# Performance work log

Hardware: AMD Instinct MI355X
Metric: run time of the kernel (lower is better)

## Reference

```python
import jax, jax.numpy as jnp
import numpy as np

T = 36
N_POLES = 40
LAM = 0.1
MAX_ITER = 100
TOL = 1e-4
B, P = 2, 4096


def build_dictionary(Drr, Dtheta):
    # rows i = 0..T-1; columns: [rr^i cos(i th), (-rr)^i cos(i th), rr^i sin(i th), (-rr)^i sin(i th)]
    i = jnp.arange(T, dtype=Drr.dtype)[:, None]              # [T,1]
    pr = jnp.power(Drr[None, :], i)                          # rr^i   [T,N]
    sign = jnp.power(jnp.asarray(-1.0, Drr.dtype), i)        # (-1)^i [T,1]
    c = jnp.cos(i * Dtheta[None, :])
    s = jnp.sin(i * Dtheta[None, :])
    dic = jnp.concatenate([pr * c, sign * pr * c, pr * s, sign * pr * s], axis=1)  # [T,4N]
    G = jnp.linalg.norm(dic, axis=0)                         # column norms
    G = jnp.where(G == 0, jnp.sqrt(jnp.asarray(float(T), dic.dtype)), G)
    return dic / G


def soft_shrink(v, lambd):
    return jnp.sign(v) * jnp.maximum(jnp.abs(v) - lambd, 0.0)


def fista(D, Y, lam, max_iter=MAX_ITER):
    DtD = D.T @ D                                            # [4N,4N]
    L = jnp.linalg.norm(DtD)                                 # torch.norm(DtD, 2) = Frobenius norm
    linv = 1.0 / L
    DtY = jnp.einsum('tk,btp->bkp', D, Y) * linv             # [B,4N,P]
    K = DtD.shape[0]
    A = jnp.eye(K, dtype=D.dtype) - DtD * linv               # [4N,4N]
    lambd = lam * linv
    Bb, _, Pp = DtY.shape

    # FISTA momentum coefficients are data independent -> precompute
    ts = np.ones(max_iter + 1)
    for k in range(max_iter):
        ts[k + 1] = (1 + np.sqrt(1 + 4 * ts[k] ** 2)) / 2.0
    tts = jnp.asarray((ts[:-1] - 1) / ts[1:], dtype=D.dtype)  # [max_iter]

    x0 = jnp.zeros((Bb, K, Pp), dtype=D.dtype)

    def step(carry, inputs):
        x_old, y_old, done = carry
        tt, k = inputs
        x_new = soft_shrink(jnp.einsum('kj,bjp->bkp', A, y_old) + DtY, lambd)
        y_new = x_new * (1 + tt) - x_old * tt
        # torch divides by x_old.shape[1]: P on the first check (x_old is the 2-D zeros init), 4N after
        denom = jnp.where(k == 0, float(Pp), float(K)).astype(x_new.dtype)
        conv = jnp.linalg.norm(x_old - x_new) / denom < TOL
        x_out = jnp.where(done, x_old, x_new)
        y_out = jnp.where(done, y_old, y_new)
        return (x_out, y_out, jnp.logical_or(done, conv)), None

    (x_fin, _, _), _ = jax.lax.scan(step, (x0, x0, jnp.array(False)),
                                    (tts, jnp.arange(max_iter)))
    return x_fin


def setup_inputs() -> dict:
    key = jax.random.key(0)
    k1, k2, k3 = jax.random.split(key, 3)
    Drr = jax.random.uniform(k1, (N_POLES,), dtype=jnp.float32)
    Dtheta = jax.random.uniform(k2, (N_POLES,), dtype=jnp.float32)
    x = jax.random.normal(k3, (B, T, P), dtype=jnp.float32)
    return {"Drr": Drr, "Dtheta": Dtheta, "x": x}


def reference(Drr, Dtheta, x):
    dic = build_dictionary(Drr, Dtheta)   # [T, 4N]
    sparsecode = fista(dic, x, LAM)       # [B, 4N, P]
    return sparsecode
```

## Files before the change

kernel.cpp:

```cpp
#include <hip/hip_runtime.h>
#include <hip/hip_fp16.h>

#define TT 36
#define KK 160
#define NPOLE 40
#define PP 4096
#define MAXIT 100
#define COLS 16
#define NG 2
#define NWC 4
#define NTHR 512
#define YS 168
#define GRID 256

#define WS_TTS   2
#define WS_ROWN  160
#define WS_D     512
#define WS_A     6400

typedef float    floatx4 __attribute__((ext_vector_type(4)));
typedef _Float16 halfx8  __attribute__((ext_vector_type(8)));

__global__ __launch_bounds__(256)
void setup_kernel(const float* __restrict__ Drr, const float* __restrict__ Dth,
                  float* __restrict__ ws) {
  __shared__ float Dl[TT * KK];
  __shared__ float red[256];
  const int a = blockIdx.x, tid = threadIdx.x;

  if (tid < KK) {
    int gg = tid / NPOLE, n = tid % NPOLE;
    float rr = Drr[n], th = Dth[n];
    float srr = (gg & 1) ? -rr : rr;
    float sth, cth; __sincosf(th, &sth, &cth);
    float c = 1.f, s = 0.f, pr = 1.f, ss = 0.f;
    for (int t = 0; t < TT; t++) {
      float val = pr * ((gg < 2) ? c : s);
      Dl[t * KK + tid] = val;
      ss = fmaf(val, val, ss);
      float cn = c * cth - s * sth;
      float sn = s * cth + c * sth;
      c = cn; s = sn; pr *= srr;
    }
    float gn = sqrtf(ss);
    gn = (gn == 0.f) ? sqrtf((float)TT) : gn;
    float inv = 1.f / gn;
    for (int t = 0; t < TT; t++) Dl[t * KK + tid] *= inv;
  }
  if (a == 0 && tid == 0) {
    double ts = 1.0;
    for (int k = 0; k < MAXIT; k++) {
      double tn = (1.0 + sqrt(1.0 + 4.0 * ts * ts)) * 0.5;
      ws[WS_TTS + k] = (float)((ts - 1.0) / tn);
      ts = tn;
    }
  }
  __syncthreads();

  if (a == 0)
    for (int idx = tid; idx < TT * KK; idx += 256) ws[WS_D + idx] = Dl[idx];

  float ss2 = 0.f;
  if (tid < KK) {
    float s2 = 0.f;
    for (int t = 0; t < TT; t++) s2 = fmaf(Dl[t * KK + a], Dl[t * KK + tid], s2);
    ws[WS_A + a * KK + tid] = s2;
    ss2 = s2 * s2;
  }
  red[tid] = ss2;
  __syncthreads();
  for (int off = 128; off > 0; off >>= 1) {
    if (tid < off) red[tid] += red[tid + off];
    __syncthreads();
  }
  if (tid == 0) ws[WS_ROWN + a] = red[0];
}

__global__ __launch_bounds__(NTHR, 2)
void fista_kernel(const float* __restrict__ x, float* __restrict__ out,
                  const float* __restrict__ ws) {
  __shared__ __align__(16) short ys[NG][2][COLS * YS];
  __shared__ float ttsl[MAXIT];
  __shared__ unsigned cnt[NG];

  const int tid  = threadIdx.x;
  const int w    = tid >> 6;
  const int lane = tid & 63;
  const int quad = lane >> 4;
  const int l16  = lane & 15;
  const int g    = w >> 2;
  const int v    = w & 3;
  const int bid  = blockIdx.x;
  const int bb   = (bid * 32) / PP;
  const int p0   = (bid * 32) % PP + 16 * g;

  float frob = 0.f;
  {
    const float* rn = &ws[WS_ROWN];
#pragma unroll
    for (int i = 0; i < KK; i += 4) {
      float4 r4 = *(const float4*)&rn[i];
      frob += ((r4.x + r4.y) + r4.z) + r4.w;
    }
  }
  const float linv  = 1.0f / sqrtf(frob);
  const float lambd = 0.1f * linv;
  const float adiag = 1.0f - linv;
  const float ahf   = (float)(_Float16)adiag;
  const float ddiag = adiag - ahf;

  int base, nrs;
  if (g == 0) { base = (v < 2) ? 48 * v : 32 * v + 32; nrs = (v < 2) ? 3 : 2; }
  else        { base = (v < 2) ? 32 * v : 48 * v - 32; nrs = (v < 2) ? 2 : 3; }

  for (int i = tid; i < MAXIT; i += NTHR) ttsl[i] = ws[WS_TTS + i];

  const float* DtDw = &ws[WS_A];
  halfx8 ah[3][5];
#pragma unroll
  for (int rs = 0; rs < 3; rs++) {
    if (rs < nrs) {
      const int myrow = base + 16 * rs + l16;
      const float* rowp = &DtDw[myrow * KK];
#pragma unroll
      for (int kc = 0; kc < 5; kc++) {
        float4 d0 = *(const float4*)&rowp[32 * kc + 8 * quad];
        float4 d1 = *(const float4*)&rowp[32 * kc + 8 * quad + 4];
        float vals[8] = {d0.x, d0.y, d0.z, d0.w, d1.x, d1.y, d1.z, d1.w};
        union { halfx8 v8; _Float16 h8[8]; } fr;
#pragma unroll
        for (int e = 0; e < 8; e++) {
          int kpos = 32 * kc + 8 * quad + e;
          float aval = (kpos == myrow) ? adiag : (-vals[e] * linv);
          fr.h8[e] = (_Float16)aval;
        }
        ah[rs][kc] = fr.v8;
      }
    }
  }

  const float* Dg = &ws[WS_D];
  float dty[3][4] = {{0.f,0.f,0.f,0.f},{0.f,0.f,0.f,0.f},{0.f,0.f,0.f,0.f}};
  {
    const float* xcol = &x[(size_t)bb * TT * PP + p0 + l16];
    for (int t = 0; t < TT; t++) {
      float xv = xcol[(size_t)t * PP];
#pragma unroll
      for (int rs = 0; rs < 3; rs++) {
        if (rs < nrs) {
          float4 d = *(const float4*)&Dg[t * KK + base + 16 * rs + 4 * quad];
          dty[rs][0] = fmaf(d.x, xv, dty[rs][0]);
          dty[rs][1] = fmaf(d.y, xv, dty[rs][1]);
          dty[rs][2] = fmaf(d.z, xv, dty[rs][2]);
          dty[rs][3] = fmaf(d.w, xv, dty[rs][3]);
        }
      }
    }
#pragma unroll
    for (int rs = 0; rs < 3; rs++)
#pragma unroll
      for (int r = 0; r < 4; r++) dty[rs][r] *= linv;
  }

  {
    int* z = (int*)&ys[0][0][0];
    for (int i = tid; i < NG * 2 * COLS * YS / 2; i += NTHR) z[i] = 0;
    if (tid < NG) cnt[tid] = 0;
  }
  float xo[3][4] = {{0.f,0.f,0.f,0.f},{0.f,0.f,0.f,0.f},{0.f,0.f,0.f,0.f}};
  float yl[3][4] = {{0.f,0.f,0.f,0.f},{0.f,0.f,0.f,0.f},{0.f,0.f,0.f,0.f}};
  float yv[3][4] = {{0.f,0.f,0.f,0.f},{0.f,0.f,0.f,0.f},{0.f,0.f,0.f,0.f}};
  __syncthreads();

  if (g == 1) __builtin_amdgcn_s_sleep(10);
  __builtin_amdgcn_s_setprio(1);

#define RD_MFMA(KC) { \
    halfx8 bh = *(const halfx8*)&yb[cb + 32 * (KC)]; \
    _Pragma("unroll") \
    for (int rs = 0; rs < 3; rs++) \
      if (rs < nrs) \
        accM[rs] = __builtin_amdgcn_mfma_f32_16x16x32_f16(ah[rs][KC], bh, accM[rs], 0, 0, 0); \
  }

#define ITER_BODY(SK, K1, K2, K3, K4) { \
    RD_MFMA(SK) \
    if (it > 0) { \
      const unsigned tgt = (unsigned)(NWC * it); \
      __builtin_amdgcn_s_setprio(0); \
      while (__atomic_load_n(&cnt[g], __ATOMIC_ACQUIRE) < tgt) \
        __builtin_amdgcn_s_sleep(1); \
      __builtin_amdgcn_s_setprio(1); \
    } \
    RD_MFMA(K1) RD_MFMA(K2) RD_MFMA(K3) RD_MFMA(K4) \
  }

  for (int it = 0; it < MAXIT; it++) {
    const short* yb = &ys[g][it & 1][0];
    const int cb = l16 * YS + 8 * quad;
    floatx4 accM[3] = {{dty[0][0], dty[0][1], dty[0][2], dty[0][3]},
                       {dty[1][0], dty[1][1], dty[1][2], dty[1][3]},
                       {dty[2][0], dty[2][1], dty[2][2], dty[2][3]}};

    if (g == 0) {
      if      (v == 0) ITER_BODY(0, 1, 2, 3, 4)
      else if (v == 1) ITER_BODY(2, 0, 1, 3, 4)
      else if (v == 2) ITER_BODY(3, 0, 1, 2, 4)
      else             ITER_BODY(4, 0, 1, 2, 3)
    } else {
      if      (v == 0) ITER_BODY(0, 1, 2, 3, 4)
      else if (v == 1) ITER_BODY(1, 0, 2, 3, 4)
      else if (v == 2) ITER_BODY(2, 0, 1, 3, 4)
      else             ITER_BODY(4, 0, 1, 2, 3)
    }

    const float tt = ttsl[it];
    short* yw = &ys[g][(it & 1) ^ 1][0];
#pragma unroll
    for (int rs = 0; rs < 3; rs++) {
      if (rs < nrs) {
        float yn[4];
#pragma unroll
        for (int r = 0; r < 4; r++) {
          float vv = fmaf(ddiag, yv[rs][r], fmaf(ahf, yl[rs][r], accM[rs][r]));
          float cl = __builtin_amdgcn_fmed3f(vv, -lambd, lambd);
          float xv = vv - cl;
          yn[r] = fmaf(tt, xv - xo[rs][r], xv);
          xo[rs][r] = xv;
        }
        _Float16 h0 = (_Float16)yn[0], h1 = (_Float16)yn[1];
        _Float16 h2 = (_Float16)yn[2], h3 = (_Float16)yn[3];
        yl[rs][0] = yn[0] - (float)h0;  yv[rs][0] = yn[0];
        yl[rs][1] = yn[1] - (float)h1;  yv[rs][1] = yn[1];
        yl[rs][2] = yn[2] - (float)h2;  yv[rs][2] = yn[2];
        yl[rs][3] = yn[3] - (float)h3;  yv[rs][3] = yn[3];
        unsigned u01 = (unsigned)__builtin_bit_cast(unsigned short, h0) |
                       ((unsigned)__builtin_bit_cast(unsigned short, h1) << 16);
        unsigned u23 = (unsigned)__builtin_bit_cast(unsigned short, h2) |
                       ((unsigned)__builtin_bit_cast(unsigned short, h3) << 16);
        const int ko = l16 * YS + base + 16 * rs + 4 * quad;
        *(uint2*)&yw[ko] = make_uint2(u01, u23);
      }
    }

    if (lane == 0) __atomic_fetch_add(&cnt[g], 1u, __ATOMIC_RELEASE);
  }

#pragma unroll
  for (int rs = 0; rs < 3; rs++) {
    if (rs < nrs) {
#pragma unroll
      for (int r = 0; r < 4; r++)
        out[((size_t)bb * KK + base + 16 * rs + 4 * quad + r) * PP + p0 + l16] = xo[rs][r];
    }
  }
}

extern "C" void kernel_launch(void* const* d_in, const int* in_sizes, int n_in,
                              void* d_out, int out_size, void* d_ws, size_t ws_size,
                              hipStream_t stream) {
  const float* Drr = (const float*)d_in[0];
  const float* Dth = (const float*)d_in[1];
  const float* x   = (const float*)d_in[2];
  float* out = (float*)d_out;
  float* ws  = (float*)d_ws;
  (void)in_sizes; (void)n_in; (void)out_size; (void)ws_size;

  setup_kernel<<<160, 256, 0, stream>>>(Drr, Dth, ws);
  fista_kernel<<<GRID, NTHR, 0, stream>>>(x, out, ws);
}
```

Measured before the change: 171.7 us.

## Fuse dictionary and Gram setup into FISTA kernel with MFMA Gram computation

Removes the separate setup kernel and its global workspace round-trip. Each block now builds the dictionary in shared memory and computes D^T D with split hi/lo fp16 MFMAs. It derives the Frobenius norm from that product, and the momentum coefficients are passed as a host-computed kernel argument. The iteration is reformulated to keep raw DtD (zero diagonal) in fp16, apply the diagonal term in fp32, and drop the fp16 residual (yl) correction of y. Every block repeats the setup work, the much larger shared-memory footprint may cut blocks per CU, and accuracy may shift.

```diff
diff --git a/kernel.cpp b/kernel.cpp
--- a/kernel.cpp
+++ b/kernel.cpp
@@ -1,5 +1,6 @@
 #include <hip/hip_runtime.h>
 #include <hip/hip_fp16.h>
+#include <cmath>
 
 #define TT 36
 #define KK 160
@@ -12,76 +13,44 @@
 #define NTHR 512
 #define YS 168
 #define GRID 256
-
-#define WS_TTS   2
-#define WS_ROWN  160
-#define WS_D     512
-#define WS_A     6400
+#define TW 64
+#define AW 168
+
+#define OFF_TH 23040
+#define OFF_TL 43520
+#define OFF_A  64000
+#define SM_SZ  117760
 
 typedef float    floatx4 __attribute__((ext_vector_type(4)));
 typedef _Float16 halfx8  __attribute__((ext_vector_type(8)));
 
-__global__ __launch_bounds__(256)
-void setup_kernel(const float* __restrict__ Drr, const float* __restrict__ Dth,
-                  float* __restrict__ ws) {
-  __shared__ float Dl[TT * KK];
-  __shared__ float red[256];
-  const int a = blockIdx.x, tid = threadIdx.x;
-
-  if (tid < KK) {
-    int gg = tid / NPOLE, n = tid % NPOLE;
-    float rr = Drr[n], th = Dth[n];
-    float srr = (gg & 1) ? -rr : rr;
-    float sth, cth; __sincosf(th, &sth, &cth);
-    float c = 1.f, s = 0.f, pr = 1.f, ss = 0.f;
-    for (int t = 0; t < TT; t++) {
-      float val = pr * ((gg < 2) ? c : s);
-      Dl[t * KK + tid] = val;
-      ss = fmaf(val, val, ss);
-      float cn = c * cth - s * sth;
-      float sn = s * cth + c * sth;
-      c = cn; s = sn; pr *= srr;
-    }
-    float gn = sqrtf(ss);
-    gn = (gn == 0.f) ? sqrtf((float)TT) : gn;
-    float inv = 1.f / gn;
-    for (int t = 0; t < TT; t++) Dl[t * KK + tid] *= inv;
-  }
-  if (a == 0 && tid == 0) {
-    double ts = 1.0;
-    for (int k = 0; k < MAXIT; k++) {
-      double tn = (1.0 + sqrt(1.0 + 4.0 * ts * ts)) * 0.5;
-      ws[WS_TTS + k] = (float)((ts - 1.0) / tn);
-      ts = tn;
-    }
-  }
-  __syncthreads();
-
-  if (a == 0)
-    for (int idx = tid; idx < TT * KK; idx += 256) ws[WS_D + idx] = Dl[idx];
-
-  float ss2 = 0.f;
-  if (tid < KK) {
-    float s2 = 0.f;
-    for (int t = 0; t < TT; t++) s2 = fmaf(Dl[t * KK + a], Dl[t * KK + tid], s2);
-    ws[WS_A + a * KK + tid] = s2;
-    ss2 = s2 * s2;
-  }
-  red[tid] = ss2;
-  __syncthreads();
-  for (int off = 128; off > 0; off >>= 1) {
-    if (tid < off) red[tid] += red[tid + off];
-    __syncthreads();
-  }
-  if (tid == 0) ws[WS_ROWN + a] = red[0];
+struct TtsArg { float v[MAXIT]; };
+
+static TtsArg host_tts() {
+  TtsArg a;
+  double ts = 1.0;
+  for (int k = 0; k < MAXIT; k++) {
+    double tn = (1.0 + sqrt(1.0 + 4.0 * ts * ts)) * 0.5;
+    a.v[k] = (float)((ts - 1.0) / tn);
+    ts = tn;
+  }
+  return a;
 }
 
 __global__ __launch_bounds__(NTHR, 2)
-void fista_kernel(const float* __restrict__ x, float* __restrict__ out,
-                  const float* __restrict__ ws) {
-  __shared__ __align__(16) short ys[NG][2][COLS * YS];
+void fista_kernel(const float* __restrict__ Drr, const float* __restrict__ Dth,
+                  const float* __restrict__ x, float* __restrict__ out,
+                  TtsArg targ) {
+  __shared__ __align__(16) char smem[SM_SZ];
   __shared__ float ttsl[MAXIT];
+  __shared__ float red[8];
   __shared__ unsigned cnt[NG];
+
+  float*    rawD = (float*)smem;
+  _Float16* Th   = (_Float16*)(smem + OFF_TH);
+  _Float16* Tl   = (_Float16*)(smem + OFF_TL);
+  _Float16* Ah   = (_Float16*)(smem + OFF_A);
+  short*    ysb  = (short*)smem;
 
   const int tid  = threadIdx.x;
   const int w    = tid >> 6;
@@ -94,52 +63,43 @@
   const int bb   = (bid * 32) / PP;
   const int p0   = (bid * 32) % PP + 16 * g;
 
-  float frob = 0.f;
-  {
-    const float* rn = &ws[WS_ROWN];
-#pragma unroll
-    for (int i = 0; i < KK; i += 4) {
-      float4 r4 = *(const float4*)&rn[i];
-      frob += ((r4.x + r4.y) + r4.z) + r4.w;
-    }
-  }
-  const float linv  = 1.0f / sqrtf(frob);
-  const float lambd = 0.1f * linv;
-  const float adiag = 1.0f - linv;
-  const float ahf   = (float)(_Float16)adiag;
-  const float ddiag = adiag - ahf;
-
   int base, nrs;
   if (g == 0) { base = (v < 2) ? 48 * v : 32 * v + 32; nrs = (v < 2) ? 3 : 2; }
   else        { base = (v < 2) ? 32 * v : 48 * v - 32; nrs = (v < 2) ? 2 : 3; }
 
-  for (int i = tid; i < MAXIT; i += NTHR) ttsl[i] = ws[WS_TTS + i];
-
-  const float* DtDw = &ws[WS_A];
-  halfx8 ah[3][5];
-#pragma unroll
-  for (int rs = 0; rs < 3; rs++) {
-    if (rs < nrs) {
-      const int myrow = base + 16 * rs + l16;
-      const float* rowp = &DtDw[myrow * KK];
-#pragma unroll
-      for (int kc = 0; kc < 5; kc++) {
-        float4 d0 = *(const float4*)&rowp[32 * kc + 8 * quad];
-        float4 d1 = *(const float4*)&rowp[32 * kc + 8 * quad + 4];
-        float vals[8] = {d0.x, d0.y, d0.z, d0.w, d1.x, d1.y, d1.z, d1.w};
-        union { halfx8 v8; _Float16 h8[8]; } fr;
-#pragma unroll
-        for (int e = 0; e < 8; e++) {
-          int kpos = 32 * kc + 8 * quad + e;
-          float aval = (kpos == myrow) ? adiag : (-vals[e] * linv);
-          fr.h8[e] = (_Float16)aval;
-        }
-        ah[rs][kc] = fr.v8;
-      }
-    }
-  }
-
-  const float* Dg = &ws[WS_D];
+  for (int i = tid; i < MAXIT; i += NTHR) ttsl[i] = targ.v[i];
+
+  if (tid < KK) {
+    int gg = tid / NPOLE, n = tid % NPOLE;
+    float rr = Drr[n], th = Dth[n];
+    float srr = (gg & 1) ? -rr : rr;
+    float sth, cth; __sincosf(th, &sth, &cth);
+    float c = 1.f, s = 0.f, pr = 1.f, ss = 0.f;
+    for (int t = 0; t < TT; t++) {
+      float val = pr * ((gg < 2) ? c : s);
+      rawD[t * KK + tid] = val;
+      ss = fmaf(val, val, ss);
+      float cn = c * cth - s * sth;
+      float sn = s * cth + c * sth;
+      c = cn; s = sn; pr *= srr;
+    }
+    float gn = sqrtf(ss);
+    gn = (gn == 0.f) ? sqrtf((float)TT) : gn;
+    float inv = 1.f / gn;
+    for (int t = 0; t < TT; t++) {
+      float d = rawD[t * KK + tid] * inv;
+      rawD[t * KK + tid] = d;
+      _Float16 h = (_Float16)d;
+      Th[tid * TW + t] = h;
+      Tl[tid * TW + t] = (_Float16)(d - (float)h);
+    }
+    for (int t = TT; t < TW; t++) {
+      Th[tid * TW + t] = (_Float16)0.f;
+      Tl[tid * TW + t] = (_Float16)0.f;
+    }
+  }
+  __syncthreads();
+
   float dty[3][4] = {{0.f,0.f,0.f,0.f},{0.f,0.f,0.f,0.f},{0.f,0.f,0.f,0.f}};
   {
     const float* xcol = &x[(size_t)bb * TT * PP + p0 + l16];
@@ -148,7 +108,7 @@
 #pragma unroll
       for (int rs = 0; rs < 3; rs++) {
         if (rs < nrs) {
-          float4 d = *(const float4*)&Dg[t * KK + base + 16 * rs + 4 * quad];
+          float4 d = *(const float4*)&rawD[t * KK + base + 16 * rs + 4 * quad];
           dty[rs][0] = fmaf(d.x, xv, dty[rs][0]);
           dty[rs][1] = fmaf(d.y, xv, dty[rs][1]);
           dty[rs][2] = fmaf(d.z, xv, dty[rs][2]);
@@ -159,16 +119,60 @@
 #pragma unroll
     for (int rs = 0; rs < 3; rs++)
 #pragma unroll
-      for (int r = 0; r < 4; r++) dty[rs][r] *= linv;
+      for (int r = 0; r < 4; r++) dty[rs][r] = -dty[rs][r];
+  }
+
+  float fpart = 0.f;
+  for (int tix = w; tix < 100; tix += 8) {
+    int i = tix / 10, j = tix % 10;
+    floatx4 acc = {0.f, 0.f, 0.f, 0.f};
+#pragma unroll
+    for (int ks = 0; ks < 2; ks++) {
+      halfx8 Ah8 = *(const halfx8*)&Th[(16 * i + l16) * TW + 32 * ks + 8 * quad];
+      halfx8 Al8 = *(const halfx8*)&Tl[(16 * i + l16) * TW + 32 * ks + 8 * quad];
+      halfx8 Bh8 = *(const halfx8*)&Th[(16 * j + l16) * TW + 32 * ks + 8 * quad];
+      halfx8 Bl8 = *(const halfx8*)&Tl[(16 * j + l16) * TW + 32 * ks + 8 * quad];
+      acc = __builtin_amdgcn_mfma_f32_16x16x32_f16(Ah8, Bh8, acc, 0, 0, 0);
+      acc = __builtin_amdgcn_mfma_f32_16x16x32_f16(Ah8, Bl8, acc, 0, 0, 0);
+      acc = __builtin_amdgcn_mfma_f32_16x16x32_f16(Al8, Bh8, acc, 0, 0, 0);
+    }
+#pragma unroll
+    for (int r = 0; r < 4; r++) {
+      float cv = acc[r];
+      fpart += cv * cv;
+      int grow = 16 * i + 4 * quad + r, gcol = 16 * j + l16;
+      Ah[grow * AW + gcol] = (_Float16)((grow == gcol) ? 0.f : cv);
+    }
+  }
+#pragma unroll
+  for (int off = 32; off > 0; off >>= 1) fpart += __shfl_xor(fpart, off);
+  if (lane == 0) red[w] = fpart;
+  __syncthreads();
+
+  const float frob = ((((((red[0] + red[1]) + red[2]) + red[3]) + red[4])
+                       + red[5]) + red[6]) + red[7];
+  const float linv  = 1.0f / sqrtf(frob);
+  const float nlinv = -linv;
+  const float lambd = 0.1f * linv;
+  const float adiag = 1.0f - linv;
+
+  halfx8 ah[3][5];
+#pragma unroll
+  for (int rs = 0; rs < 3; rs++) {
+    if (rs < nrs) {
+      const int myrow = base + 16 * rs + l16;
+#pragma unroll
+      for (int kc = 0; kc < 5; kc++)
+        ah[rs][kc] = *(const halfx8*)&Ah[myrow * AW + 32 * kc + 8 * quad];
+    }
   }
 
   {
-    int* z = (int*)&ys[0][0][0];
+    int* z = (int*)ysb;
     for (int i = tid; i < NG * 2 * COLS * YS / 2; i += NTHR) z[i] = 0;
     if (tid < NG) cnt[tid] = 0;
   }
   float xo[3][4] = {{0.f,0.f,0.f,0.f},{0.f,0.f,0.f,0.f},{0.f,0.f,0.f,0.f}};
-  float yl[3][4] = {{0.f,0.f,0.f,0.f},{0.f,0.f,0.f,0.f},{0.f,0.f,0.f,0.f}};
   float yv[3][4] = {{0.f,0.f,0.f,0.f},{0.f,0.f,0.f,0.f},{0.f,0.f,0.f,0.f}};
   __syncthreads();
 
@@ -196,7 +200,7 @@
   }
 
   for (int it = 0; it < MAXIT; it++) {
-    const short* yb = &ys[g][it & 1][0];
+    const short* yb = ysb + (2 * g + (it & 1)) * (COLS * YS);
     const int cb = l16 * YS + 8 * quad;
     floatx4 accM[3] = {{dty[0][0], dty[0][1], dty[0][2], dty[0][3]},
                        {dty[1][0], dty[1][1], dty[1][2], dty[1][3]},
@@ -215,25 +219,22 @@
     }
 
     const float tt = ttsl[it];
-    short* yw = &ys[g][(it & 1) ^ 1][0];
+    short* yw = ysb + (2 * g + ((it & 1) ^ 1)) * (COLS * YS);
 #pragma unroll
     for (int rs = 0; rs < 3; rs++) {
       if (rs < nrs) {
         float yn[4];
 #pragma unroll
         for (int r = 0; r < 4; r++) {
-          float vv = fmaf(ddiag, yv[rs][r], fmaf(ahf, yl[rs][r], accM[rs][r]));
+          float vv = fmaf(nlinv, accM[rs][r], adiag * yv[rs][r]);
           float cl = __builtin_amdgcn_fmed3f(vv, -lambd, lambd);
           float xv = vv - cl;
           yn[r] = fmaf(tt, xv - xo[rs][r], xv);
           xo[rs][r] = xv;
+          yv[rs][r] = yn[r];
         }
         _Float16 h0 = (_Float16)yn[0], h1 = (_Float16)yn[1];
         _Float16 h2 = (_Float16)yn[2], h3 = (_Float16)yn[3];
-        yl[rs][0] = yn[0] - (float)h0;  yv[rs][0] = yn[0];
-        yl[rs][1] = yn[1] - (float)h1;  yv[rs][1] = yn[1];
-        yl[rs][2] = yn[2] - (float)h2;  yv[rs][2] = yn[2];
-        yl[rs][3] = yn[3] - (float)h3;  yv[rs][3] = yn[3];
         unsigned u01 = (unsigned)__builtin_bit_cast(unsigned short, h0) |
                        ((unsigned)__builtin_bit_cast(unsigned short, h1) << 16);
         unsigned u23 = (unsigned)__builtin_bit_cast(unsigned short, h2) |
@@ -263,9 +264,7 @@
   const float* Dth = (const float*)d_in[1];
   const float* x   = (const float*)d_in[2];
   float* out = (float*)d_out;
-  float* ws  = (float*)d_ws;
-  (void)in_sizes; (void)n_in; (void)out_size; (void)ws_size;
-
-  setup_kernel<<<160, 256, 0, stream>>>(Drr, Dth, ws);
-  fista_kernel<<<GRID, NTHR, 0, stream>>>(x, out, ws);
+  (void)d_ws; (void)ws_size; (void)in_sizes; (void)n_in; (void)out_size;
+
+  fista_kernel<<<GRID, NTHR, 0, stream>>>(Drr, Dth, x, out, host_tts());
 }
```

Measured after the change: 181.4 us. 5.7% more time.

## Precompute fp16 off-diagonal DtD, fold scaling into epilogue, pass tts as kernel arg

Applied to the files above, without the earlier changes.

Setup now stores DtD directly as fp16 with a zeroed diagonal, so the fista kernel loads A fragments without per-thread conversion. The iteration is rewritten as v = adiag*y - linv*(DtD_off*y - DtY): the diagonal is applied exactly in fp32 from the held y values, which replaces the hi/lo split compensation and drops the yl registers and several FMAs per element. The momentum coefficients are computed on the host and passed by value as a kernel argument, and buffers move from the workspace to __device__ globals. The fp16 rounding now applies to unscaled DtD entries, which changes the numerics, and the work removed from the hot loop is small.

```diff
diff --git a/kernel.cpp b/kernel.cpp
--- a/kernel.cpp
+++ b/kernel.cpp
@@ -1,5 +1,6 @@
 #include <hip/hip_runtime.h>
 #include <hip/hip_fp16.h>
+#include <cmath>
 
 #define TT 36
 #define KK 160
@@ -13,17 +14,28 @@
 #define YS 168
 #define GRID 256
 
-#define WS_TTS   2
-#define WS_ROWN  160
-#define WS_D     512
-#define WS_A     6400
-
 typedef float    floatx4 __attribute__((ext_vector_type(4)));
 typedef _Float16 halfx8  __attribute__((ext_vector_type(8)));
 
+__device__ __align__(16) float    g_D[TT * KK];
+__device__ __align__(16) float    g_rown[KK];
+__device__ __align__(16) _Float16 g_A[KK * KK];
+
+struct TtsArg { float v[MAXIT]; };
+
+static TtsArg host_tts() {
+  TtsArg a;
+  double ts = 1.0;
+  for (int k = 0; k < MAXIT; k++) {
+    double tn = (1.0 + sqrt(1.0 + 4.0 * ts * ts)) * 0.5;
+    a.v[k] = (float)((ts - 1.0) / tn);
+    ts = tn;
+  }
+  return a;
+}
+
 __global__ __launch_bounds__(256)
-void setup_kernel(const float* __restrict__ Drr, const float* __restrict__ Dth,
-                  float* __restrict__ ws) {
+void setup_kernel(const float* __restrict__ Drr, const float* __restrict__ Dth) {
   __shared__ float Dl[TT * KK];
   __shared__ float red[256];
   const int a = blockIdx.x, tid = threadIdx.x;
@@ -47,24 +59,16 @@
     float inv = 1.f / gn;
     for (int t = 0; t < TT; t++) Dl[t * KK + tid] *= inv;
   }
-  if (a == 0 && tid == 0) {
-    double ts = 1.0;
-    for (int k = 0; k < MAXIT; k++) {
-      double tn = (1.0 + sqrt(1.0 + 4.0 * ts * ts)) * 0.5;
-      ws[WS_TTS + k] = (float)((ts - 1.0) / tn);
-      ts = tn;
-    }
-  }
   __syncthreads();
 
   if (a == 0)
-    for (int idx = tid; idx < TT * KK; idx += 256) ws[WS_D + idx] = Dl[idx];
+    for (int idx = tid; idx < TT * KK; idx += 256) g_D[idx] = Dl[idx];
 
   float ss2 = 0.f;
   if (tid < KK) {
     float s2 = 0.f;
     for (int t = 0; t < TT; t++) s2 = fmaf(Dl[t * KK + a], Dl[t * KK + tid], s2);
-    ws[WS_A + a * KK + tid] = s2;
+    g_A[a * KK + tid] = (_Float16)((tid == a) ? 0.f : s2);
     ss2 = s2 * s2;
   }
   red[tid] = ss2;
@@ -73,12 +77,12 @@
     if (tid < off) red[tid] += red[tid + off];
     __syncthreads();
   }
-  if (tid == 0) ws[WS_ROWN + a] = red[0];
+  if (tid == 0) g_rown[a] = red[0];
 }
 
 __global__ __launch_bounds__(NTHR, 2)
 void fista_kernel(const float* __restrict__ x, float* __restrict__ out,
-                  const float* __restrict__ ws) {
+                  TtsArg targ) {
   __shared__ __align__(16) short ys[NG][2][COLS * YS];
   __shared__ float ttsl[MAXIT];
   __shared__ unsigned cnt[NG];
@@ -95,51 +99,33 @@
   const int p0   = (bid * 32) % PP + 16 * g;
 
   float frob = 0.f;
-  {
-    const float* rn = &ws[WS_ROWN];
-#pragma unroll
-    for (int i = 0; i < KK; i += 4) {
-      float4 r4 = *(const float4*)&rn[i];
-      frob += ((r4.x + r4.y) + r4.z) + r4.w;
-    }
+#pragma unroll
+  for (int i = 0; i < KK; i += 4) {
+    float4 r4 = *(const float4*)&g_rown[i];
+    frob += ((r4.x + r4.y) + r4.z) + r4.w;
   }
   const float linv  = 1.0f / sqrtf(frob);
+  const float nlinv = -linv;
   const float lambd = 0.1f * linv;
   const float adiag = 1.0f - linv;
-  const float ahf   = (float)(_Float16)adiag;
-  const float ddiag = adiag - ahf;
 
   int base, nrs;
   if (g == 0) { base = (v < 2) ? 48 * v : 32 * v + 32; nrs = (v < 2) ? 3 : 2; }
   else        { base = (v < 2) ? 32 * v : 48 * v - 32; nrs = (v < 2) ? 2 : 3; }
 
-  for (int i = tid; i < MAXIT; i += NTHR) ttsl[i] = ws[WS_TTS + i];
-
-  const float* DtDw = &ws[WS_A];
+  for (int i = tid; i < MAXIT; i += NTHR) ttsl[i] = targ.v[i];
+
   halfx8 ah[3][5];
 #pragma unroll
   for (int rs = 0; rs < 3; rs++) {
     if (rs < nrs) {
       const int myrow = base + 16 * rs + l16;
-      const float* rowp = &DtDw[myrow * KK];
-#pragma unroll
-      for (int kc = 0; kc < 5; kc++) {
-        float4 d0 = *(const float4*)&rowp[32 * kc + 8 * quad];
-        float4 d1 = *(const float4*)&rowp[32 * kc + 8 * quad + 4];
-        float vals[8] = {d0.x, d0.y, d0.z, d0.w, d1.x, d1.y, d1.z, d1.w};
-        union { halfx8 v8; _Float16 h8[8]; } fr;
-#pragma unroll
-        for (int e = 0; e < 8; e++) {
-          int kpos = 32 * kc + 8 * quad + e;
-          float aval = (kpos == myrow) ? adiag : (-vals[e] * linv);
-          fr.h8[e] = (_Float16)aval;
-        }
-        ah[rs][kc] = fr.v8;
-      }
-    }
-  }
-
-  const float* Dg = &ws[WS_D];
+#pragma unroll
+      for (int kc = 0; kc < 5; kc++)
+        ah[rs][kc] = *(const halfx8*)&g_A[myrow * KK + 32 * kc + 8 * quad];
+    }
+  }
+
   float dty[3][4] = {{0.f,0.f,0.f,0.f},{0.f,0.f,0.f,0.f},{0.f,0.f,0.f,0.f}};
   {
     const float* xcol = &x[(size_t)bb * TT * PP + p0 + l16];
@@ -148,7 +134,7 @@
 #pragma unroll
       for (int rs = 0; rs < 3; rs++) {
         if (rs < nrs) {
-          float4 d = *(const float4*)&Dg[t * KK + base + 16 * rs + 4 * quad];
+          float4 d = *(const float4*)&g_D[t * KK + base + 16 * rs + 4 * quad];
           dty[rs][0] = fmaf(d.x, xv, dty[rs][0]);
           dty[rs][1] = fmaf(d.y, xv, dty[rs][1]);
           dty[rs][2] = fmaf(d.z, xv, dty[rs][2]);
@@ -159,7 +145,7 @@
 #pragma unroll
     for (int rs = 0; rs < 3; rs++)
 #pragma unroll
-      for (int r = 0; r < 4; r++) dty[rs][r] *= linv;
+      for (int r = 0; r < 4; r++) dty[rs][r] = -dty[rs][r];
   }
 
   {
@@ -168,7 +154,6 @@
     if (tid < NG) cnt[tid] = 0;
   }
   float xo[3][4] = {{0.f,0.f,0.f,0.f},{0.f,0.f,0.f,0.f},{0.f,0.f,0.f,0.f}};
-  float yl[3][4] = {{0.f,0.f,0.f,0.f},{0.f,0.f,0.f,0.f},{0.f,0.f,0.f,0.f}};
   float yv[3][4] = {{0.f,0.f,0.f,0.f},{0.f,0.f,0.f,0.f},{0.f,0.f,0.f,0.f}};
   __syncthreads();
 
@@ -222,18 +207,15 @@
         float yn[4];
 #pragma unroll
         for (int r = 0; r < 4; r++) {
-          float vv = fmaf(ddiag, yv[rs][r], fmaf(ahf, yl[rs][r], accM[rs][r]));
+          float vv = fmaf(nlinv, accM[rs][r], adiag * yv[rs][r]);
           float cl = __builtin_amdgcn_fmed3f(vv, -lambd, lambd);
           float xv = vv - cl;
           yn[r] = fmaf(tt, xv - xo[rs][r], xv);
           xo[rs][r] = xv;
+          yv[rs][r] = yn[r];
         }
         _Float16 h0 = (_Float16)yn[0], h1 = (_Float16)yn[1];
         _Float16 h2 = (_Float16)yn[2], h3 = (_Float16)yn[3];
-        yl[rs][0] = yn[0] - (float)h0;  yv[rs][0] = yn[0];
-        yl[rs][1] = yn[1] - (float)h1;  yv[rs][1] = yn[1];
-        yl[rs][2] = yn[2] - (float)h2;  yv[rs][2] = yn[2];
-        yl[rs][3] = yn[3] - (float)h3;  yv[rs][3] = yn[3];
         unsigned u01 = (unsigned)__builtin_bit_cast(unsigned short, h0) |
                        ((unsigned)__builtin_bit_cast(unsigned short, h1) << 16);
         unsigned u23 = (unsigned)__builtin_bit_cast(unsigned short, h2) |
@@ -263,9 +245,8 @@
   const float* Dth = (const float*)d_in[1];
   const float* x   = (const float*)d_in[2];
   float* out = (float*)d_out;
-  float* ws  = (float*)d_ws;
-  (void)in_sizes; (void)n_in; (void)out_size; (void)ws_size;
-
-  setup_kernel<<<160, 256, 0, stream>>>(Drr, Dth, ws);
-  fista_kernel<<<GRID, NTHR, 0, stream>>>(x, out, ws);
-}
+  (void)d_ws; (void)ws_size; (void)in_sizes; (void)n_in; (void)out_size;
+
+  setup_kernel<<<160, 256, 0, stream>>>(Drr, Dth);
+  fista_kernel<<<GRID, NTHR, 0, stream>>>(x, out, host_tts());
+}
```

Result: faster. 152.8 us (median of 3 runs) (-11.0%).
